# Performance work log

Hardware: AMD Instinct MI355X
Metric: run time of the kernel (lower is better)

## Reference

```python
import jax, jax.numpy as jnp
import numpy as np
from jax import lax

HEATMAP_THRESH = 0.1


def _conv(x, w, b, stride=1):
    y = lax.conv_general_dilated(x, w, (stride, stride), 'SAME',
                                 dimension_numbers=('NCHW', 'OIHW', 'NCHW'))
    return y + b[None, :, None, None]


def _maxpool2(x):
    return lax.reduce_window(x, -jnp.inf, lax.max, (1, 1, 2, 2), (1, 1, 2, 2), 'VALID')


def _up2(x):
    return jnp.repeat(jnp.repeat(x, 2, axis=2), 2, axis=3)


def _find_peaks_mask(hm, thresh):
    # Vectorized equivalent of the CPU nested-loop _find_peaks:
    # interior pixel is a peak iff v > thresh and v >= its 4 axial neighbors.
    c = hm[:, :, 1:-1, 1:-1]
    m = ((c > thresh)
         & (c >= hm[:, :, :-2, 1:-1]) & (c >= hm[:, :, 2:, 1:-1])
         & (c >= hm[:, :, 1:-1, :-2]) & (c >= hm[:, :, 1:-1, 2:]))
    return jnp.pad(m, ((0, 0), (0, 0), (1, 1), (1, 1)))  # border never a peak


def _param(key, shape):
    fan_in = int(np.prod(shape[1:]))
    return jax.random.normal(key, shape, jnp.float32) / np.sqrt(fan_in)


_SHAPES = {
    'w_d1': (32, 3, 3, 3), 'w_d2': (64, 32, 3, 3), 'w_bn': (128, 64, 3, 3),
    'w_u1': (64, 192, 3, 3), 'w_u2': (32, 96, 3, 3), 'w_seg': (1, 32, 1, 1),
    'w_p1': (64, 4, 3, 3), 'w_p2': (128, 64, 3, 3),
    'w_hm': (17, 128, 1, 1), 'w_paf': (32, 128, 1, 1),
}


def setup_inputs() -> dict:
    key = jax.random.key(0)
    ks = jax.random.split(key, 1 + len(_SHAPES))
    B, H, W = 8, 384, 384
    inp = {'x': jax.random.normal(ks[0], (B, 3, H, W), jnp.float32)}
    for i, (n, s) in enumerate(_SHAPES.items()):
        inp[n] = _param(ks[i + 1], s)
        inp[n.replace('w_', 'b_')] = jnp.zeros((s[0],), jnp.float32)
    return inp


def _forward(x, w_d1, b_d1, w_d2, b_d2, w_bn, b_bn, w_u1, b_u1, w_u2, b_u2,
             w_seg, b_seg, w_p1, b_p1, w_p2, b_p2, w_hm, b_hm, w_paf, b_paf):
    # --- UNet segmentation ---
    d1 = jax.nn.relu(_conv(x, w_d1, b_d1))                    # [B,32,384,384]
    d2 = jax.nn.relu(_conv(_maxpool2(d1), w_d2, b_d2))        # [B,64,192,192]
    bn = jax.nn.relu(_conv(_maxpool2(d2), w_bn, b_bn))        # [B,128,96,96]
    u1 = jax.nn.relu(_conv(jnp.concatenate([_up2(bn), d2], 1), w_u1, b_u1))  # [B,64,192,192]
    u2 = jax.nn.relu(_conv(jnp.concatenate([_up2(u1), d1], 1), w_u2, b_u2))  # [B,32,384,384]
    seg = _conv(u2, w_seg, b_seg)                             # [B,1,384,384]
    # --- Pose net on image + detached seg logits ---
    xp = jnp.concatenate([x, lax.stop_gradient(seg)], axis=1)  # detach()
    p1 = jax.nn.relu(_conv(xp, w_p1, b_p1, stride=2))          # [B,64,192,192]
    p2 = jax.nn.relu(_conv(p1, w_p2, b_p2, stride=2))          # [B,128,96,96]
    hm = _conv(p2, w_hm, b_hm)                                 # [B,17,96,96]
    paf = _conv(p2, w_paf, b_paf)                              # [B,32,96,96]
    return seg, hm, paf


def reference(x, w_d1, b_d1, w_d2, b_d2, w_bn, b_bn, w_u1, b_u1, w_u2, b_u2,
              w_seg, b_seg, w_p1, b_p1, w_p2, b_p2, w_hm, b_hm, w_paf, b_paf):
    seg, hm, paf = _forward(x, w_d1, b_d1, w_d2, b_d2, w_bn, b_bn, w_u1, b_u1,
                            w_u2, b_u2, w_seg, b_seg, w_p1, b_p1, w_p2, b_p2,
                            w_hm, b_hm, w_paf, b_paf)
    # jit-friendly replacement for the variable-length python peak lists:
    # boolean mask over [B,K,h,w]; (x,y) coords recoverable via jnp.nonzero offline.
    peaks = _find_peaks_mask(hm, HEATMAP_THRESH)
    return seg, hm, paf, peaks
```

## Files before the change

kernel.cpp:

```cpp
#include <hip/hip_runtime.h>


#define BS 256

typedef _Float16 half8 __attribute__((ext_vector_type(8)));
typedef float floatx4 __attribute__((ext_vector_type(4)));

#define LDSDW 20
#define PLT 6000

__global__ __launch_bounds__(BS) void packw_gen_kernel(
    const float* __restrict__ w, _Float16* __restrict__ bp, int Cin, int Cout)
{
    int total = (Cin >> 5) * 9 * (Cout >> 4) * 64;
    int tid = blockIdx.x * BS + threadIdx.x;
    if (tid >= total) return;
    int lane = tid & 63;
    int t = tid >> 6;
    int NTl = Cout >> 4;
    int nt = t % NTl; t /= NTl;
    int tap = t % 9;
    int chunk = t / 9;
    int q = lane >> 4, n = lane & 15;
    int co = nt * 16 + n;
    _Float16* ph = bp + (size_t)tid * 8;
    _Float16* pl = bp + (size_t)total * 8 + (size_t)tid * 8;
#pragma unroll
    for (int j = 0; j < 8; ++j) {
        int ci = chunk * 32 + q * 8 + j;
        float v = w[((size_t)co * Cin + ci) * 9 + tap];
        _Float16 h = (_Float16)v;
        ph[j] = h;
        pl[j] = (_Float16)(v - (float)h);
    }
}

__global__ __launch_bounds__(BS) void packw_1x1_kernel(
    const float* __restrict__ w, _Float16* __restrict__ bp, int Cin, int NTl, int Cout)
{
    int total = (Cin >> 5) * NTl * 64;
    int tid = blockIdx.x * BS + threadIdx.x;
    if (tid >= total) return;
    int lane = tid & 63;
    int t = tid >> 6;
    int nt = t % NTl;
    int chunk = t / NTl;
    int q = lane >> 4, n = lane & 15;
    int co = nt * 16 + n;
    _Float16* ph = bp + (size_t)tid * 8;
    _Float16* pl = bp + (size_t)total * 8 + (size_t)tid * 8;
#pragma unroll
    for (int j = 0; j < 8; ++j) {
        int ci = chunk * 32 + q * 8 + j;
        float v = (co < Cout) ? w[(size_t)co * Cin + ci] : 0.f;
        _Float16 h = (_Float16)v;
        ph[j] = h;
        pl[j] = (_Float16)(v - (float)h);
    }
}

template <int CHUNKS, int NT, int HH, int WW>
__global__ __launch_bounds__(BS) void conv3x3_mfma_kernel(
    const float* __restrict__ in_,
    const _Float16* __restrict__ bp,
    const float* __restrict__ bias,
    float* __restrict__ out)
{
    constexpr int PL = 4 * 34 * LDSDW;
    constexpr int EPI = 64 * NT * 16;
    constexpr int LDS_DW = (2 * PL > EPI) ? 2 * PL : EPI;
    __shared__ unsigned int lds[LDS_DW];

    int xblks = WW / 32;
    int b = blockIdx.x;
    int xb = b % xblks; b /= xblks;
    int yp = b % (HH / 2);
    int n  = b / (HH / 2);
    int y0 = yp * 2;
    int x0 = xb * 32;

    int tid = threadIdx.x;
    int lane = tid & 63, wv = tid >> 6;
    int m = lane & 15, q = lane >> 4;
    int lrow = wv >> 1;
    int lx   = (wv & 1) * 16;

    floatx4 acc[NT];
#pragma unroll
    for (int nt = 0; nt < NT; ++nt) acc[nt] = (floatx4){0.f, 0.f, 0.f, 0.f};

    const int planeW = CHUNKS * 9 * NT * 64 * 8;

    for (int chunk = 0; chunk < CHUNKS; ++chunk) {
        __syncthreads();
        for (int e = tid; e < 4 * 34 * 4; e += BS) {
            int xi = e % 34;
            int rest = e / 34;
            int oct = rest & 3;
            int row = rest >> 2;
            int iy = y0 - 1 + row, gx = x0 - 1 + xi;
            bool ok = (iy >= 0 && iy < HH && gx >= 0 && gx < WW);
            const float* gp = in_ +
                ((size_t)(n * (CHUNKS * 32) + chunk * 32 + oct * 8) * HH + iy) * WW + gx;
            half8 hv, lv;
#pragma unroll
            for (int j = 0; j < 8; ++j) {
                float v = ok ? gp[(size_t)j * HH * WW] : 0.f;
                _Float16 h = (_Float16)v;
                hv[j] = h;
                lv[j] = (_Float16)(v - (float)h);
            }
            int base = (row * 34 + xi) * LDSDW + oct * 4;
            *(half8*)((char*)lds + (size_t)base * 4) = hv;
            *(half8*)((char*)lds + ((size_t)PL + base) * 4) = lv;
        }
        __syncthreads();
#pragma unroll
        for (int ky = 0; ky < 3; ++ky) {
#pragma unroll
            for (int kx = 0; kx < 3; ++kx) {
                int row = lrow + ky;
                int xi  = lx + m + kx;
                int adw = (row * 34 + xi) * LDSDW + q * 4;
                half8 ah = *(const half8*)((const char*)lds + (size_t)adw * 4);
                half8 al = *(const half8*)((const char*)lds + ((size_t)PL + adw) * 4);
                int tap = ky * 3 + kx;
                const _Float16* bpp = bp + ((size_t)(chunk * 9 + tap) * NT) * 64 * 8;
#pragma unroll
                for (int nt = 0; nt < NT; ++nt) {
                    half8 bh = *(const half8*)(bpp + ((size_t)nt * 64 + lane) * 8);
                    half8 bl = *(const half8*)(bpp + planeW + ((size_t)nt * 64 + lane) * 8);
                    acc[nt] = __builtin_amdgcn_mfma_f32_16x16x32_f16(ah, bh, acc[nt], 0, 0, 0);
                    acc[nt] = __builtin_amdgcn_mfma_f32_16x16x32_f16(ah, bl, acc[nt], 0, 0, 0);
                    acc[nt] = __builtin_amdgcn_mfma_f32_16x16x32_f16(al, bh, acc[nt], 0, 0, 0);
                }
            }
        }
    }

    __syncthreads();
#pragma unroll
    for (int nt = 0; nt < NT; ++nt) {
#pragma unroll
        for (int r = 0; r < 4; ++r) {
            int co = nt * 16 + m;
            int pxl = wv * 16 + q * 4 + r;
            ((float*)lds)[co * 64 + pxl] = acc[nt][r];
        }
    }
    __syncthreads();
    {
        constexpr int thPerCo = 256 / (NT * 16);
        constexpr int pxPerTh = 64 / thPerCo;
        int co = tid / thPerCo;
        int sub = tid % thPerCo;
        int pxb = sub * pxPerTh;
        float bb = bias[co];
#pragma unroll
        for (int u = 0; u < pxPerTh; u += 4) {
            int p = pxb + u;
            int row = y0 + (p >> 5), xx = x0 + (p & 31);
            const float* lp = (const float*)lds + co * 64 + p;
            float4 vv = *(const float4*)lp;
            vv.x = fmaxf(vv.x + bb, 0.f);
            vv.y = fmaxf(vv.y + bb, 0.f);
            vv.z = fmaxf(vv.z + bb, 0.f);
            vv.w = fmaxf(vv.w + bb, 0.f);
            *(float4*)(out + ((size_t)(n * NT * 16 + co) * HH + row) * WW + xx) = vv;
        }
    }
}

template <int CHUNKS, int NT, int WI>
__global__ __launch_bounds__(BS) void conv3x3s2_mfma_kernel(
    const float* __restrict__ in_,
    const _Float16* __restrict__ bp,
    const float* __restrict__ bias,
    float* __restrict__ out)
{
    constexpr int WO = WI / 2;
    constexpr int PLs = 5 * 68 * LDSDW;
    constexpr int EPI = 64 * NT * 16;
    constexpr int LDS_DW = (2 * PLs > EPI) ? 2 * PLs : EPI;
    __shared__ unsigned int lds[LDS_DW];

    int xblks = WO / 32;
    int b = blockIdx.x;
    int xb = b % xblks; b /= xblks;
    int yp = b % (WO / 2);
    int n  = b / (WO / 2);
    int y0 = yp * 2;
    int x0 = xb * 32;

    int tid = threadIdx.x;
    int lane = tid & 63, wv = tid >> 6;
    int m = lane & 15, q = lane >> 4;
    int lrow = wv >> 1;
    int lx   = (wv & 1) * 16;

    floatx4 acc[NT];
#pragma unroll
    for (int nt = 0; nt < NT; ++nt) acc[nt] = (floatx4){0.f, 0.f, 0.f, 0.f};

    const int planeW = CHUNKS * 9 * NT * 64 * 8;

    for (int chunk = 0; chunk < CHUNKS; ++chunk) {
        __syncthreads();
        for (int e = tid; e < 5 * 68 * 4; e += BS) {
            int xi = e % 68;
            int rest = e / 68;
            int oct = rest & 3;
            int row = rest >> 2;
            int iy = 2 * y0 + row, ix = 2 * x0 + xi;
            bool ok = (xi < 65 && iy < WI && ix < WI);
            const float* gp = in_ +
                ((size_t)(n * (CHUNKS * 32) + chunk * 32 + oct * 8) * WI + iy) * WI + ix;
            half8 hv, lv;
#pragma unroll
            for (int j = 0; j < 8; ++j) {
                float v = ok ? gp[(size_t)j * WI * WI] : 0.f;
                _Float16 h = (_Float16)v;
                hv[j] = h;
                lv[j] = (_Float16)(v - (float)h);
            }
            int pos = (xi & 1) * 34 + (xi >> 1);
            int base = (row * 68 + pos) * LDSDW + oct * 4;
            *(half8*)((char*)lds + (size_t)base * 4) = hv;
            *(half8*)((char*)lds + ((size_t)PLs + base) * 4) = lv;
        }
        __syncthreads();
#pragma unroll
        for (int ky = 0; ky < 3; ++ky) {
#pragma unroll
            for (int kx = 0; kx < 3; ++kx) {
                int row = 2 * lrow + ky;
                int pos = (kx & 1) * 34 + (lx + m) + (kx >> 1);
                int adw = (row * 68 + pos) * LDSDW + q * 4;
                half8 ah = *(const half8*)((const char*)lds + (size_t)adw * 4);
                half8 al = *(const half8*)((const char*)lds + ((size_t)PLs + adw) * 4);
                int tap = ky * 3 + kx;
                const _Float16* bpp = bp + ((size_t)(chunk * 9 + tap) * NT) * 64 * 8;
#pragma unroll
                for (int nt = 0; nt < NT; ++nt) {
                    half8 bh = *(const half8*)(bpp + ((size_t)nt * 64 + lane) * 8);
                    half8 bl = *(const half8*)(bpp + planeW + ((size_t)nt * 64 + lane) * 8);
                    acc[nt] = __builtin_amdgcn_mfma_f32_16x16x32_f16(ah, bh, acc[nt], 0, 0, 0);
                    acc[nt] = __builtin_amdgcn_mfma_f32_16x16x32_f16(ah, bl, acc[nt], 0, 0, 0);
                    acc[nt] = __builtin_amdgcn_mfma_f32_16x16x32_f16(al, bh, acc[nt], 0, 0, 0);
                }
            }
        }
    }

    __syncthreads();
#pragma unroll
    for (int nt = 0; nt < NT; ++nt) {
#pragma unroll
        for (int r = 0; r < 4; ++r) {
            int co = nt * 16 + m;
            int pxl = wv * 16 + q * 4 + r;
            ((float*)lds)[co * 64 + pxl] = acc[nt][r];
        }
    }
    __syncthreads();
    {
        constexpr int thPerCo = 256 / (NT * 16);
        constexpr int pxPerTh = 64 / thPerCo;
        int co = tid / thPerCo;
        int sub = tid % thPerCo;
        int pxb = sub * pxPerTh;
        float bb = bias[co];
#pragma unroll
        for (int u = 0; u < pxPerTh; u += 4) {
            int p = pxb + u;
            int row = y0 + (p >> 5), xx = x0 + (p & 31);
            const float* lp = (const float*)lds + co * 64 + p;
            float4 vv = *(const float4*)lp;
            vv.x = fmaxf(vv.x + bb, 0.f);
            vv.y = fmaxf(vv.y + bb, 0.f);
            vv.z = fmaxf(vv.z + bb, 0.f);
            vv.w = fmaxf(vv.w + bb, 0.f);
            *(float4*)(out + ((size_t)(n * NT * 16 + co) * WO + row) * WO + xx) = vv;
        }
    }
}

template <int CHUNKS, int NT>
__global__ __launch_bounds__(BS) void conv1x1_mfma_kernel(
    const float* __restrict__ in_,
    const _Float16* __restrict__ bp,
    const float* __restrict__ bias,
    float* __restrict__ out,
    int Cout, int HW)
{
    constexpr int PL1 = 64 * LDSDW;
    constexpr int EPI = 64 * NT * 16;
    constexpr int LDS_DW = (2 * PL1 > EPI) ? 2 * PL1 : EPI;
    __shared__ unsigned int lds[LDS_DW];

    int pblks = HW / 64;
    int b = blockIdx.x;
    int pb = b % pblks;
    int n  = b / pblks;
    int sp0 = pb * 64;

    int tid = threadIdx.x;
    int lane = tid & 63, wv = tid >> 6;
    int m = lane & 15, q = lane >> 4;

    floatx4 acc[NT];
#pragma unroll
    for (int nt = 0; nt < NT; ++nt) acc[nt] = (floatx4){0.f, 0.f, 0.f, 0.f};

    const int planeW = CHUNKS * NT * 64 * 8;

    for (int chunk = 0; chunk < CHUNKS; ++chunk) {
        __syncthreads();
        {
            int px = tid & 63;
            int oct = tid >> 6;
            const float* gp = in_ +
                ((size_t)(n * (CHUNKS * 32) + chunk * 32 + oct * 8)) * HW + sp0 + px;
            half8 hv, lv;
#pragma unroll
            for (int j = 0; j < 8; ++j) {
                float v = gp[(size_t)j * HW];
                _Float16 h = (_Float16)v;
                hv[j] = h;
                lv[j] = (_Float16)(v - (float)h);
            }
            int base = px * LDSDW + oct * 4;
            *(half8*)((char*)lds + (size_t)base * 4) = hv;
            *(half8*)((char*)lds + ((size_t)PL1 + base) * 4) = lv;
        }
        __syncthreads();
        {
            int adw = (wv * 16 + m) * LDSDW + q * 4;
            half8 ah = *(const half8*)((const char*)lds + (size_t)adw * 4);
            half8 al = *(const half8*)((const char*)lds + ((size_t)PL1 + adw) * 4);
            const _Float16* bpp = bp + ((size_t)chunk * NT) * 64 * 8;
#pragma unroll
            for (int nt = 0; nt < NT; ++nt) {
                half8 bh = *(const half8*)(bpp + ((size_t)nt * 64 + lane) * 8);
                half8 bl = *(const half8*)(bpp + planeW + ((size_t)nt * 64 + lane) * 8);
                acc[nt] = __builtin_amdgcn_mfma_f32_16x16x32_f16(ah, bh, acc[nt], 0, 0, 0);
                acc[nt] = __builtin_amdgcn_mfma_f32_16x16x32_f16(ah, bl, acc[nt], 0, 0, 0);
                acc[nt] = __builtin_amdgcn_mfma_f32_16x16x32_f16(al, bh, acc[nt], 0, 0, 0);
            }
        }
    }

    __syncthreads();
#pragma unroll
    for (int nt = 0; nt < NT; ++nt) {
#pragma unroll
        for (int r = 0; r < 4; ++r) {
            ((float*)lds)[(nt * 16 + m) * 64 + wv * 16 + q * 4 + r] = acc[nt][r];
        }
    }
    __syncthreads();
    {
        constexpr int thPerCo = 256 / (NT * 16);
        constexpr int pxPerTh = 64 / thPerCo;
        int co = tid / thPerCo;
        int g  = tid % thPerCo;
        if (co < Cout) {
            float bb = bias[co];
            const float* lp = (const float*)lds + co * 64 + g * pxPerTh;
            float* op = out + ((size_t)(n * Cout + co)) * HW + sp0 + g * pxPerTh;
#pragma unroll
            for (int u = 0; u < pxPerTh; u += 4) {
                float4 vv = *(const float4*)(lp + u);
                vv.x += bb; vv.y += bb; vv.z += bb; vv.w += bb;
                *(float4*)(op + u) = vv;
            }
        }
    }
}

__global__ __launch_bounds__(BS) void u1_mfma_kernel(
    const float* __restrict__ bn_,
    const float* __restrict__ d2_,
    const _Float16* __restrict__ bp,
    const float* __restrict__ b_u1,
    float* __restrict__ out)
{
    __shared__ unsigned int lds[2 * PLT];
    const int Ho = 192, Wo = 192;
    int b = blockIdx.x;
    int xb = b % 4; b /= 4;
    int yb = b % 48;
    int n  = b / 48;
    int y0 = yb * 4;
    int x0 = xb * 48;

    int tid = threadIdx.x;
    int lane = tid & 63, wv = tid >> 6;
    int m = lane & 15, q = lane >> 4;
    int yr = y0 + wv;

    floatx4 acc[3][4];
#pragma unroll
    for (int mt = 0; mt < 3; ++mt)
#pragma unroll
        for (int nt = 0; nt < 4; ++nt) acc[mt][nt] = (floatx4){0.f, 0.f, 0.f, 0.f};

    const int hh0 = (y0 - 1) >> 1;
    const int hx0 = (x0 - 1) >> 1;

    for (int chunk = 0; chunk < 6; ++chunk) {
        __syncthreads();
        if (chunk < 4) {
            for (int e = tid; e < 4 * 26 * 4; e += BS) {
                int xi = e % 26;
                int rest = e / 26;
                int oct = rest & 3;
                int row = rest >> 2;
                int hy = hh0 + row, hx = hx0 + xi;
                bool ok = (hy >= 0 && hy < 96 && hx >= 0 && hx < 96);
                const float* gp = bn_ +
                    ((size_t)(n * 128 + chunk * 32 + oct * 8) * 96 + hy) * 96 + hx;
                half8 hv, lv;
#pragma unroll
                for (int j = 0; j < 8; ++j) {
                    float v = ok ? gp[(size_t)j * 96 * 96] : 0.f;
                    _Float16 h = (_Float16)v;
                    hv[j] = h;
                    lv[j] = (_Float16)(v - (float)h);
                }
                int base = (row * 50 + xi) * LDSDW + oct * 4;
                *(half8*)((char*)lds + (size_t)base * 4) = hv;
                *(half8*)((char*)lds + ((size_t)PLT + base) * 4) = lv;
            }
        } else {
            for (int e = tid; e < 6 * 50 * 4; e += BS) {
                int xi = e % 50;
                int rest = e / 50;
                int oct = rest & 3;
                int row = rest >> 2;
                int iy = y0 - 1 + row, gx = x0 - 1 + xi;
                bool ok = (iy >= 0 && iy < Ho && gx >= 0 && gx < Wo);
                const float* gp = d2_ +
                    ((size_t)(n * 64 + (chunk - 4) * 32 + oct * 8) * Ho + iy) * Wo + gx;
                half8 hv, lv;
#pragma unroll
                for (int j = 0; j < 8; ++j) {
                    float v = ok ? gp[(size_t)j * Ho * Wo] : 0.f;
                    _Float16 h = (_Float16)v;
                    hv[j] = h;
                    lv[j] = (_Float16)(v - (float)h);
                }
                int base = (row * 50 + xi) * LDSDW + oct * 4;
                *(half8*)((char*)lds + (size_t)base * 4) = hv;
                *(half8*)((char*)lds + ((size_t)PLT + base) * 4) = lv;
            }
        }
        __syncthreads();
#pragma unroll
        for (int ky = 0; ky < 3; ++ky) {
#pragma unroll
            for (int kx = 0; kx < 3; ++kx) {
                int tap = ky * 3 + kx;
                const _Float16* bpp = bp + ((size_t)(chunk * 9 + tap) * 4) * 64 * 8;
                half8 bh[4], bl[4];
#pragma unroll
                for (int nt = 0; nt < 4; ++nt) {
                    bh[nt] = *(const half8*)(bpp + ((size_t)nt * 64 + lane) * 8);
                    bl[nt] = *(const half8*)(bpp + 110592 + ((size_t)nt * 64 + lane) * 8);
                }
                int row;
                if (chunk < 4) row = ((yr + ky - 1) >> 1) - hh0;
                else           row = wv + ky;
#pragma unroll
                for (int mt = 0; mt < 3; ++mt) {
                    int px = 16 * mt + m;
                    int xi = (chunk < 4) ? (((x0 + px + kx - 1) >> 1) - hx0)
                                         : (px + kx);
                    int adw = (row * 50 + xi) * LDSDW + q * 4;
                    half8 ah = *(const half8*)((const char*)lds + (size_t)adw * 4);
                    half8 al = *(const half8*)((const char*)lds + ((size_t)PLT + adw) * 4);
#pragma unroll
                    for (int nt = 0; nt < 4; ++nt) {
                        acc[mt][nt] = __builtin_amdgcn_mfma_f32_16x16x32_f16(ah, bh[nt], acc[mt][nt], 0, 0, 0);
                        acc[mt][nt] = __builtin_amdgcn_mfma_f32_16x16x32_f16(ah, bl[nt], acc[mt][nt], 0, 0, 0);
                        acc[mt][nt] = __builtin_amdgcn_mfma_f32_16x16x32_f16(al, bh[nt], acc[mt][nt], 0, 0, 0);
                    }
                }
            }
        }
    }

#pragma unroll
    for (int h = 0; h < 2; ++h) {
        __syncthreads();
#pragma unroll
        for (int ntl = 0; ntl < 2; ++ntl) {
#pragma unroll
            for (int mt = 0; mt < 3; ++mt) {
#pragma unroll
                for (int r = 0; r < 4; ++r) {
                    ((float*)lds)[(ntl * 16 + m) * 192 + wv * 48 + 16 * mt + q * 4 + r]
                        = acc[mt][h * 2 + ntl][r];
                }
            }
        }
        __syncthreads();
        {
            int col = tid >> 3;
            int g   = tid & 7;
            int row = g >> 1, xx = (g & 1) * 24;
            int co = h * 32 + col;
            float bb = b_u1[co];
            const float* lp = (const float*)lds + col * 192 + g * 24;
            float* op = out + ((size_t)(n * 64 + co) * Ho + y0 + row) * Wo + x0 + xx;
#pragma unroll
            for (int u = 0; u < 24; u += 4) {
                float4 vv = *(const float4*)(lp + u);
                vv.x = fmaxf(vv.x + bb, 0.f);
                vv.y = fmaxf(vv.y + bb, 0.f);
                vv.z = fmaxf(vv.z + bb, 0.f);
                vv.w = fmaxf(vv.w + bb, 0.f);
                *(float4*)(op + u) = vv;
            }
        }
    }
}

__global__ __launch_bounds__(BS) void u2seg_mfma_kernel(
    const float* __restrict__ u1_,
    const float* __restrict__ d1_,
    const _Float16* __restrict__ bp,
    const float* __restrict__ b_u2,
    const float* __restrict__ w_seg,
    const float* __restrict__ b_seg,
    float* __restrict__ seg)
{
    __shared__ unsigned int lds[2 * PLT];
    const int Ho = 384, Wo = 384;
    int b = blockIdx.x;
    int xb = b % 8; b /= 8;
    int yb = b % 96;
    int n  = b / 96;
    int y0 = yb * 4;
    int x0 = xb * 48;

    int tid = threadIdx.x;
    int lane = tid & 63, wv = tid >> 6;
    int m = lane & 15, q = lane >> 4;
    int yr = y0 + wv;

    floatx4 acc[3][2];
#pragma unroll
    for (int mt = 0; mt < 3; ++mt) {
        acc[mt][0] = (floatx4){0.f, 0.f, 0.f, 0.f};
        acc[mt][1] = (floatx4){0.f, 0.f, 0.f, 0.f};
    }

    const int hh0 = (y0 - 1) >> 1;
    const int hx0 = (x0 - 1) >> 1;

    for (int chunk = 0; chunk < 3; ++chunk) {
        __syncthreads();
        if (chunk < 2) {
            for (int e = tid; e < 4 * 26 * 4; e += BS) {
                int xi = e % 26;
                int rest = e / 26;
                int oct = rest & 3;
                int row = rest >> 2;
                int hy = hh0 + row, hx = hx0 + xi;
                bool ok = (hy >= 0 && hy < 192 && hx >= 0 && hx < 192);
                const float* gp = u1_ +
                    ((size_t)(n * 64 + chunk * 32 + oct * 8) * 192 + hy) * 192 + hx;
                half8 hv, lv;
#pragma unroll
                for (int j = 0; j < 8; ++j) {
                    float v = ok ? gp[(size_t)j * 192 * 192] : 0.f;
                    _Float16 h = (_Float16)v;
                    hv[j] = h;
                    lv[j] = (_Float16)(v - (float)h);
                }
                int base = (row * 50 + xi) * LDSDW + oct * 4;
                *(half8*)((char*)lds + (size_t)base * 4) = hv;
                *(half8*)((char*)lds + ((size_t)PLT + base) * 4) = lv;
            }
        } else {
            for (int e = tid; e < 6 * 50 * 4; e += BS) {
                int xi = e % 50;
                int rest = e / 50;
                int oct = rest & 3;
                int row = rest >> 2;
                int iy = y0 - 1 + row, gx = x0 - 1 + xi;
                bool ok = (iy >= 0 && iy < Ho && gx >= 0 && gx < Wo);
                const float* gp = d1_ +
                    ((size_t)(n * 32 + oct * 8) * Ho + iy) * Wo + gx;
                half8 hv, lv;
#pragma unroll
                for (int j = 0; j < 8; ++j) {
                    float v = ok ? gp[(size_t)j * Ho * Wo] : 0.f;
                    _Float16 h = (_Float16)v;
                    hv[j] = h;
                    lv[j] = (_Float16)(v - (float)h);
                }
                int base = (row * 50 + xi) * LDSDW + oct * 4;
                *(half8*)((char*)lds + (size_t)base * 4) = hv;
                *(half8*)((char*)lds + ((size_t)PLT + base) * 4) = lv;
            }
        }
        __syncthreads();
#pragma unroll
        for (int ky = 0; ky < 3; ++ky) {
#pragma unroll
            for (int kx = 0; kx < 3; ++kx) {
                int tap = ky * 3 + kx;
                const _Float16* bpp = bp + ((size_t)(chunk * 9 + tap) * 2) * 64 * 8;
                half8 bh0 = *(const half8*)(bpp + (size_t)lane * 8);
                half8 bl0 = *(const half8*)(bpp + 27648 + (size_t)lane * 8);
                half8 bh1 = *(const half8*)(bpp + ((size_t)64 + lane) * 8);
                half8 bl1 = *(const half8*)(bpp + 27648 + ((size_t)64 + lane) * 8);
                int row;
                if (chunk < 2) row = ((yr + ky - 1) >> 1) - hh0;
                else           row = wv + ky;
#pragma unroll
                for (int mt = 0; mt < 3; ++mt) {
                    int px = 16 * mt + m;
                    int xi = (chunk < 2) ? (((x0 + px + kx - 1) >> 1) - hx0)
                                         : (px + kx);
                    int adw = (row * 50 + xi) * LDSDW + q * 4;
                    half8 ah = *(const half8*)((const char*)lds + (size_t)adw * 4);
                    half8 al = *(const half8*)((const char*)lds + ((size_t)PLT + adw) * 4);
                    acc[mt][0] = __builtin_amdgcn_mfma_f32_16x16x32_f16(ah, bh0, acc[mt][0], 0, 0, 0);
                    acc[mt][0] = __builtin_amdgcn_mfma_f32_16x16x32_f16(ah, bl0, acc[mt][0], 0, 0, 0);
                    acc[mt][0] = __builtin_amdgcn_mfma_f32_16x16x32_f16(al, bh0, acc[mt][0], 0, 0, 0);
                    acc[mt][1] = __builtin_amdgcn_mfma_f32_16x16x32_f16(ah, bh1, acc[mt][1], 0, 0, 0);
                    acc[mt][1] = __builtin_amdgcn_mfma_f32_16x16x32_f16(ah, bl1, acc[mt][1], 0, 0, 0);
                    acc[mt][1] = __builtin_amdgcn_mfma_f32_16x16x32_f16(al, bh1, acc[mt][1], 0, 0, 0);
                }
            }
        }
    }

    float bb0 = b_u2[m], bb1 = b_u2[16 + m];
    float ws0 = w_seg[m], ws1 = w_seg[16 + m];
    float bseg = b_seg[0];
#pragma unroll
    for (int mt = 0; mt < 3; ++mt) {
        float sr[4];
#pragma unroll
        for (int r = 0; r < 4; ++r) {
            float p = ws0 * fmaxf(acc[mt][0][r] + bb0, 0.f)
                    + ws1 * fmaxf(acc[mt][1][r] + bb1, 0.f);
            p += __shfl_xor(p, 1);
            p += __shfl_xor(p, 2);
            p += __shfl_xor(p, 4);
            p += __shfl_xor(p, 8);
            sr[r] = p + bseg;
        }
        if (m == 0) {
            float4 o; o.x = sr[0]; o.y = sr[1]; o.z = sr[2]; o.w = sr[3];
            *(float4*)(seg + ((size_t)n * Ho + yr) * Wo + x0 + 16 * mt + q * 4) = o;
        }
    }
}


template <int UPA, int TCO>
__global__ __launch_bounds__(BS, 2) void conv3x3_x8_kernel(
    const float* __restrict__ inA, int Ca,
    const float* __restrict__ inB, int Cb,
    const float* __restrict__ w, const float* __restrict__ b,
    float* __restrict__ out,
    int N, int H, int W, int Cout, int do_relu)
{
    const int W8 = W >> 3;
    int idx = blockIdx.x * BS + threadIdx.x;
    int total = N * H * W8;
    if (idx >= total) return;
    int x8 = idx % W8;
    int t  = idx / W8;
    int y  = t % H;
    int n  = t / H;
    int x0 = x8 << 3;
    const int co0 = blockIdx.y * TCO;
    const bool left_ok  = (x0 > 0);
    const bool right_ok = (x0 + 8 < W);
    const int Cin = Ca + Cb;

    float acc[TCO][8];
#pragma unroll
    for (int j = 0; j < TCO; ++j) {
        float bv = b[co0 + j];
#pragma unroll
        for (int p = 0; p < 8; ++p) acc[j][p] = bv;
    }

    for (int ci = 0; ci < Cin; ++ci) {
        float v[3][10];
#pragma unroll
        for (int ky = 0; ky < 3; ++ky) {
            int iy = y + ky - 1;
            if (iy < 0 || iy >= H) {
#pragma unroll
                for (int p = 0; p < 10; ++p) v[ky][p] = 0.f;
                continue;
            }
            if (UPA == 2 && ci < Ca) {
                const float* r = inA + ((size_t)(n * Ca + ci) * (H >> 1) + (iy >> 1)) * (W >> 1);
                int xh = x0 >> 1;
                float sm = left_ok  ? r[xh - 1] : 0.f;
                float4 qq = *(const float4*)(r + xh);
                float s4 = right_ok ? r[xh + 4] : 0.f;
                v[ky][0] = sm;
                v[ky][1] = qq.x; v[ky][2] = qq.x;
                v[ky][3] = qq.y; v[ky][4] = qq.y;
                v[ky][5] = qq.z; v[ky][6] = qq.z;
                v[ky][7] = qq.w; v[ky][8] = qq.w;
                v[ky][9] = s4;
            } else {
                const float* r = (ci < Ca)
                    ? inA + ((size_t)(n * Ca + ci) * H + iy) * W
                    : inB + ((size_t)(n * Cb + (ci - Ca)) * H + iy) * W;
                v[ky][0] = left_ok ? r[x0 - 1] : 0.f;
                float4 q0 = *(const float4*)(r + x0);
                float4 q1 = *(const float4*)(r + x0 + 4);
                v[ky][1] = q0.x; v[ky][2] = q0.y; v[ky][3] = q0.z; v[ky][4] = q0.w;
                v[ky][5] = q1.x; v[ky][6] = q1.y; v[ky][7] = q1.z; v[ky][8] = q1.w;
                v[ky][9] = right_ok ? r[x0 + 8] : 0.f;
            }
        }
#pragma unroll
        for (int j = 0; j < TCO; ++j) {
            const float* wp = w + ((size_t)(co0 + j) * Cin + ci) * 9;
#pragma unroll
            for (int ky = 0; ky < 3; ++ky) {
                float w0 = wp[ky * 3 + 0], w1 = wp[ky * 3 + 1], w2 = wp[ky * 3 + 2];
#pragma unroll
                for (int p = 0; p < 8; ++p)
                    acc[j][p] += w0 * v[ky][p] + w1 * v[ky][p + 1] + w2 * v[ky][p + 2];
            }
        }
    }

#pragma unroll
    for (int j = 0; j < TCO; ++j) {
#pragma unroll
        for (int p = 0; p < 8; ++p)
            if (do_relu) acc[j][p] = fmaxf(acc[j][p], 0.f);
        float* o = out + ((size_t)(n * Cout + co0 + j) * H + y) * W + x0;
        float4 q0; q0.x = acc[j][0]; q0.y = acc[j][1]; q0.z = acc[j][2]; q0.w = acc[j][3];
        float4 q1; q1.x = acc[j][4]; q1.y = acc[j][5]; q1.z = acc[j][6]; q1.w = acc[j][7];
        *(float4*)o = q0;
        *(float4*)(o + 4) = q1;
    }
}

template <int TCO>
__global__ __launch_bounds__(BS) void conv3x3_s2_co_kernel(
    const float* __restrict__ inA, int Ca,
    const float* __restrict__ inB, int Cb,
    const float* __restrict__ w, const float* __restrict__ b,
    float* __restrict__ out,
    int N, int Hi, int Wi, int Cout, int do_relu)
{
    const int Ho = Hi >> 1, Wo = Wi >> 1, Woq = Wo >> 2;
    int idx = blockIdx.x * BS + threadIdx.x;
    int total = N * Ho * Woq;
    if (idx >= total) return;
    int q  = idx % Woq;
    int t  = idx / Woq;
    int oy = t % Ho;
    int n  = t / Ho;
    int ox0 = q << 2;
    int ix0 = ox0 << 1;
    const int co0 = blockIdx.y * TCO;
    const bool right_ok = (ix0 + 8 < Wi);
    const int Cin = Ca + Cb;

    float acc[TCO][4];
#pragma unroll
    for (int j = 0; j < TCO; ++j) {
        float bv = b[co0 + j];
        acc[j][0] = bv; acc[j][1] = bv; acc[j][2] = bv; acc[j][3] = bv;
    }

    for (int ci = 0; ci < Cin; ++ci) {
        const float* base = (ci < Ca)
            ? inA + (size_t)(n * Ca + ci) * Hi * Wi
            : inB + (size_t)(n * Cb + (ci - Ca)) * Hi * Wi;
        float v[3][9];
#pragma unroll
        for (int ky = 0; ky < 3; ++ky) {
            int iy = 2 * oy + ky;
            if (iy >= Hi) {
#pragma unroll
                for (int p = 0; p < 9; ++p) v[ky][p] = 0.f;
                continue;
            }
            const float* r = base + (size_t)iy * Wi + ix0;
            float4 a = *(const float4*)r;
            float4 c = *(const float4*)(r + 4);
            v[ky][0] = a.x; v[ky][1] = a.y; v[ky][2] = a.z; v[ky][3] = a.w;
            v[ky][4] = c.x; v[ky][5] = c.y; v[ky][6] = c.z; v[ky][7] = c.w;
            v[ky][8] = right_ok ? r[8] : 0.f;
        }
#pragma unroll
        for (int j = 0; j < TCO; ++j) {
            const float* wp = w + ((size_t)(co0 + j) * Cin + ci) * 9;
#pragma unroll
            for (int ky = 0; ky < 3; ++ky) {
                float w0 = wp[ky * 3 + 0], w1 = wp[ky * 3 + 1], w2 = wp[ky * 3 + 2];
#pragma unroll
                for (int p = 0; p < 4; ++p)
                    acc[j][p] += w0 * v[ky][2 * p] + w1 * v[ky][2 * p + 1] + w2 * v[ky][2 * p + 2];
            }
        }
    }

#pragma unroll
    for (int j = 0; j < TCO; ++j) {
        float4 o;
        o.x = acc[j][0]; o.y = acc[j][1]; o.z = acc[j][2]; o.w = acc[j][3];
        if (do_relu) {
            o.x = fmaxf(o.x, 0.f); o.y = fmaxf(o.y, 0.f);
            o.z = fmaxf(o.z, 0.f); o.w = fmaxf(o.w, 0.f);
        }
        *(float4*)(out + ((size_t)(n * Cout + co0 + j) * Ho + oy) * Wo + ox0) = o;
    }
}

__global__ __launch_bounds__(BS) void maxpool2_kernel(
    const float* __restrict__ in, float* __restrict__ out, int NC, int H, int W)
{
    int Ho = H >> 1, Wo = W >> 1, Woq = Wo >> 2;
    int idx = blockIdx.x * BS + threadIdx.x;
    int total = NC * Ho * Woq;
    if (idx >= total) return;
    int x4 = idx % Woq;
    int t  = idx / Woq;
    int y  = t % Ho;
    int c  = t / Ho;
    const float* r0 = in + ((size_t)c * H + 2 * y) * W + 8 * x4;
    const float* r1 = r0 + W;
    float4 a0 = *(const float4*)r0;
    float4 a1 = *(const float4*)(r0 + 4);
    float4 b0 = *(const float4*)r1;
    float4 b1 = *(const float4*)(r1 + 4);
    float4 o;
    o.x = fmaxf(fmaxf(a0.x, a0.y), fmaxf(b0.x, b0.y));
    o.y = fmaxf(fmaxf(a0.z, a0.w), fmaxf(b0.z, b0.w));
    o.z = fmaxf(fmaxf(a1.x, a1.y), fmaxf(b1.x, b1.y));
    o.w = fmaxf(fmaxf(a1.z, a1.w), fmaxf(b1.z, b1.w));
    *(float4*)(out + ((size_t)c * Ho + y) * Wo + 4 * x4) = o;
}

__global__ __launch_bounds__(BS) void peaks_kernel(
    const float* __restrict__ hm, float* __restrict__ out,
    int NC, int H, int W, float thresh)
{
    int idx = blockIdx.x * BS + threadIdx.x;
    int total = NC * H * W;
    if (idx >= total) return;
    int x = idx % W;
    int t = idx / W;
    int y = t % H;
    int c = t / H;
    float r = 0.f;
    if (x >= 1 && x < W - 1 && y >= 1 && y < H - 1) {
        const float* base = hm + (size_t)c * H * W;
        float cv = base[y * W + x];
        if (cv > thresh &&
            cv >= base[(y - 1) * W + x] &&
            cv >= base[(y + 1) * W + x] &&
            cv >= base[y * W + (x - 1)] &&
            cv >= base[y * W + (x + 1)])
            r = 1.f;
    }
    out[idx] = r;
}

static inline int nblk(long n) { return (int)((n + BS - 1) / BS); }

extern "C" void kernel_launch(void* const* d_in, const int* in_sizes, int n_in,
                              void* d_out, int out_size, void* d_ws, size_t ws_size,
                              hipStream_t stream)
{
    const float* x     = (const float*)d_in[0];
    const float* w_d1  = (const float*)d_in[1];  const float* b_d1  = (const float*)d_in[2];
    const float* w_d2  = (const float*)d_in[3];  const float* b_d2  = (const float*)d_in[4];
    const float* w_bn  = (const float*)d_in[5];  const float* b_bn  = (const float*)d_in[6];
    const float* w_u1  = (const float*)d_in[7];  const float* b_u1  = (const float*)d_in[8];
    const float* w_u2  = (const float*)d_in[9];  const float* b_u2  = (const float*)d_in[10];
    const float* w_seg = (const float*)d_in[11]; const float* b_seg = (const float*)d_in[12];
    const float* w_p1  = (const float*)d_in[13]; const float* b_p1  = (const float*)d_in[14];
    const float* w_p2  = (const float*)d_in[15]; const float* b_p2  = (const float*)d_in[16];
    const float* w_hm  = (const float*)d_in[17]; const float* b_hm  = (const float*)d_in[18];
    const float* w_paf = (const float*)d_in[19]; const float* b_paf = (const float*)d_in[20];

    const int N = 8, H = 384, W = 384;
    const int H2 = 192, W2 = 192, H4 = 96, W4 = 96;

    float* ws = (float*)d_ws;
    float* u1  = ws;
    float* d1  = ws + 18874368;
    float* d2  = ws + 18874368;
    float* bn  = ws + 37748736;
    float* pd1 = ws;
    float* pd2 = ws + 47185920;
    float* p1  = ws;
    float* p2  = ws + 18874368;

    float* out_seg   = (float*)d_out;
    float* out_hm    = out_seg + 1179648;
    float* out_paf   = out_hm + 1253376;
    float* out_peaks = out_paf + 2359296;
    _Float16* bp_u1  = (_Float16*)(out_seg + 4792320);
    _Float16* bp_u2  = (_Float16*)(out_seg + 4902912);
    _Float16* bp_d2  = (_Float16*)(out_seg + 4930560);
    _Float16* bp_bn  = (_Float16*)(out_seg + 4948992);
    _Float16* bp_p2  = (_Float16*)(out_seg + 5022720);
    _Float16* bp_hm  = (_Float16*)(out_seg + 5096448);
    _Float16* bp_paf = (_Float16*)(out_seg + 5100544);

    packw_gen_kernel<<<nblk(13824), BS, 0, stream>>>(w_u1, bp_u1, 192, 64);
    packw_gen_kernel<<<nblk(3456),  BS, 0, stream>>>(w_u2, bp_u2, 96, 32);
    packw_gen_kernel<<<nblk(2304),  BS, 0, stream>>>(w_d2, bp_d2, 32, 64);
    packw_gen_kernel<<<nblk(9216),  BS, 0, stream>>>(w_bn, bp_bn, 64, 128);
    packw_gen_kernel<<<nblk(9216),  BS, 0, stream>>>(w_p2, bp_p2, 64, 128);
    packw_1x1_kernel<<<nblk(512),   BS, 0, stream>>>(w_hm, bp_hm, 128, 2, 17);
    packw_1x1_kernel<<<nblk(512),   BS, 0, stream>>>(w_paf, bp_paf, 128, 2, 32);
    {
        dim3 g(nblk((long)N * H * (W / 8)), 32 / 8);
        conv3x3_x8_kernel<1, 8><<<g, BS, 0, stream>>>(
            x, 3, nullptr, 0, w_d1, b_d1, d1, N, H, W, 32, 1);
    }
    maxpool2_kernel<<<nblk((long)N * 32 * H2 * (W2 / 4)), BS, 0, stream>>>(d1, pd1, N * 32, H, W);
    conv3x3_mfma_kernel<1, 4, 192, 192><<<8 * 96 * 6, BS, 0, stream>>>(
        pd1, bp_d2, b_d2, d2);
    maxpool2_kernel<<<nblk((long)N * 64 * H4 * (W4 / 4)), BS, 0, stream>>>(d2, pd2, N * 64, H2, W2);
    conv3x3_mfma_kernel<2, 8, 96, 96><<<8 * 48 * 3, BS, 0, stream>>>(
        pd2, bp_bn, b_bn, bn);
    u1_mfma_kernel<<<8 * 48 * 4, BS, 0, stream>>>(bn, d2, bp_u1, b_u1, u1);
    {
        dim3 g(nblk((long)N * H * (W / 8)), 32 / 8);
        conv3x3_x8_kernel<1, 8><<<g, BS, 0, stream>>>(
            x, 3, nullptr, 0, w_d1, b_d1, d1, N, H, W, 32, 1);
    }
    u2seg_mfma_kernel<<<8 * 96 * 8, BS, 0, stream>>>(
        u1, d1, bp_u2, b_u2, w_seg, b_seg, out_seg);
    {
        dim3 g(nblk((long)N * H2 * (W2 / 4)), 64 / 8);
        conv3x3_s2_co_kernel<8><<<g, BS, 0, stream>>>(
            x, 3, out_seg, 1, w_p1, b_p1, p1, N, H, W, 64, 1);
    }
    conv3x3s2_mfma_kernel<2, 8, 192><<<8 * 48 * 3, BS, 0, stream>>>(
        p1, bp_p2, b_p2, p2);
    conv1x1_mfma_kernel<4, 2><<<8 * 144, BS, 0, stream>>>(
        p2, bp_hm, b_hm, out_hm, 17, H4 * W4);
    conv1x1_mfma_kernel<4, 2><<<8 * 144, BS, 0, stream>>>(
        p2, bp_paf, b_paf, out_paf, 32, H4 * W4);
    peaks_kernel<<<nblk((long)N * 17 * H4 * W4), BS, 0, stream>>>(
        out_hm, out_peaks, N * 17, H4, W4, 0.1f);
}
```

Measured before the change: 1.013 ms.

## Store intermediate activations as pre-split fp16 hi/lo in channel-octet layout

Producer kernels (d2, bn, u1, the recomputed d1) now write their activations directly as fp16 high/low split pairs in an NC8HW8 layout. Consumer kernels then load half8 vectors instead of doing eight strided fp32 loads plus a split conversion per element. This removes redundant conversion work and uncoalesced channel-strided reads in the u1 and u2seg staging. In exchange the producer epilogues do more work, the workspace buffers are rearranged, and d2 is written twice (fp32 for maxpool and split for u1).

New measurement: 982.8 us. 1.03x faster.

```diff
diff --git a/kernel.cpp b/kernel.cpp
--- a/kernel.cpp
+++ b/kernel.cpp
@@ -59,12 +59,14 @@
     }
 }
 
-template <int CHUNKS, int NT, int HH, int WW>
+template <int CHUNKS, int NT, int HH, int WW, int OUTMODE>
 __global__ __launch_bounds__(BS) void conv3x3_mfma_kernel(
     const float* __restrict__ in_,
     const _Float16* __restrict__ bp,
     const float* __restrict__ bias,
-    float* __restrict__ out)
+    float* __restrict__ out,
+    _Float16* __restrict__ osph,
+    _Float16* __restrict__ ospl)
 {
     constexpr int PL = 4 * 34 * LDSDW;
     constexpr int EPI = 64 * NT * 16;
@@ -149,7 +151,7 @@
         }
     }
     __syncthreads();
-    {
+    if (OUTMODE != 1) {
         constexpr int thPerCo = 256 / (NT * 16);
         constexpr int pxPerTh = 64 / thPerCo;
         int co = tid / thPerCo;
@@ -169,6 +171,25 @@
             *(float4*)(out + ((size_t)(n * NT * 16 + co) * HH + row) * WW + xx) = vv;
         }
     }
+    if (OUTMODE >= 1) {
+        constexpr int OCTS = NT * 2;
+        for (int it = tid; it < OCTS * 64; it += BS) {
+            int px = it & 63;
+            int oct = it >> 6;
+            int row = y0 + (px >> 5), xx = x0 + (px & 31);
+            half8 hv, lv;
+#pragma unroll
+            for (int j = 0; j < 8; ++j) {
+                float v = fmaxf(((float*)lds)[(oct * 8 + j) * 64 + px] + bias[oct * 8 + j], 0.f);
+                _Float16 hh = (_Float16)v;
+                hv[j] = hh;
+                lv[j] = (_Float16)(v - (float)hh);
+            }
+            size_t oaddr = ((size_t)((n * OCTS + oct) * HH + row) * WW + xx) * 8;
+            *(half8*)(osph + oaddr) = hv;
+            *(half8*)(ospl + oaddr) = lv;
+        }
+    }
 }
 
 template <int CHUNKS, int NT, int WI>
@@ -379,11 +400,11 @@
 }
 
 __global__ __launch_bounds__(BS) void u1_mfma_kernel(
-    const float* __restrict__ bn_,
-    const float* __restrict__ d2_,
+    const _Float16* __restrict__ bnh, const _Float16* __restrict__ bnl,
+    const _Float16* __restrict__ d2h, const _Float16* __restrict__ d2l,
     const _Float16* __restrict__ bp,
     const float* __restrict__ b_u1,
-    float* __restrict__ out)
+    _Float16* __restrict__ oh, _Float16* __restrict__ ol_)
 {
     __shared__ unsigned int lds[2 * PLT];
     const int Ho = 192, Wo = 192;
@@ -417,16 +438,11 @@
                 int oct = rest & 3;
                 int row = rest >> 2;
                 int hy = hh0 + row, hx = hx0 + xi;
-                bool ok = (hy >= 0 && hy < 96 && hx >= 0 && hx < 96);
-                const float* gp = bn_ +
-                    ((size_t)(n * 128 + chunk * 32 + oct * 8) * 96 + hy) * 96 + hx;
-                half8 hv, lv;
-#pragma unroll
-                for (int j = 0; j < 8; ++j) {
-                    float v = ok ? gp[(size_t)j * 96 * 96] : 0.f;
-                    _Float16 h = (_Float16)v;
-                    hv[j] = h;
-                    lv[j] = (_Float16)(v - (float)h);
+                half8 hv = {}, lv = {};
+                if (hy >= 0 && hy < 96 && hx >= 0 && hx < 96) {
+                    size_t ga = ((size_t)((n * 16 + chunk * 4 + oct) * 96 + hy) * 96 + hx) * 8;
+                    hv = *(const half8*)(bnh + ga);
+                    lv = *(const half8*)(bnl + ga);
                 }
                 int base = (row * 50 + xi) * LDSDW + oct * 4;
                 *(half8*)((char*)lds + (size_t)base * 4) = hv;
@@ -439,16 +455,11 @@
                 int oct = rest & 3;
                 int row = rest >> 2;
                 int iy = y0 - 1 + row, gx = x0 - 1 + xi;
-                bool ok = (iy >= 0 && iy < Ho && gx >= 0 && gx < Wo);
-                const float* gp = d2_ +
-                    ((size_t)(n * 64 + (chunk - 4) * 32 + oct * 8) * Ho + iy) * Wo + gx;
-                half8 hv, lv;
-#pragma unroll
-                for (int j = 0; j < 8; ++j) {
-                    float v = ok ? gp[(size_t)j * Ho * Wo] : 0.f;
-                    _Float16 h = (_Float16)v;
-                    hv[j] = h;
-                    lv[j] = (_Float16)(v - (float)h);
+                half8 hv = {}, lv = {};
+                if (iy >= 0 && iy < Ho && gx >= 0 && gx < Wo) {
+                    size_t ga = ((size_t)((n * 8 + (chunk - 4) * 4 + oct) * Ho + iy) * Wo + gx) * 8;
+                    hv = *(const half8*)(d2h + ga);
+                    lv = *(const half8*)(d2l + ga);
                 }
                 int base = (row * 50 + xi) * LDSDW + oct * 4;
                 *(half8*)((char*)lds + (size_t)base * 4) = hv;
@@ -505,30 +516,29 @@
             }
         }
         __syncthreads();
-        {
-            int col = tid >> 3;
-            int g   = tid & 7;
-            int row = g >> 1, xx = (g & 1) * 24;
-            int co = h * 32 + col;
-            float bb = b_u1[co];
-            const float* lp = (const float*)lds + col * 192 + g * 24;
-            float* op = out + ((size_t)(n * 64 + co) * Ho + y0 + row) * Wo + x0 + xx;
-#pragma unroll
-            for (int u = 0; u < 24; u += 4) {
-                float4 vv = *(const float4*)(lp + u);
-                vv.x = fmaxf(vv.x + bb, 0.f);
-                vv.y = fmaxf(vv.y + bb, 0.f);
-                vv.z = fmaxf(vv.z + bb, 0.f);
-                vv.w = fmaxf(vv.w + bb, 0.f);
-                *(float4*)(op + u) = vv;
-            }
+        for (int it = tid; it < 4 * 192; it += BS) {
+            int px = it % 192;
+            int ol = it / 192;
+            int row = y0 + px / 48, xx = x0 + px % 48;
+            half8 hv, lv;
+#pragma unroll
+            for (int j = 0; j < 8; ++j) {
+                int col = ol * 8 + j;
+                float v = fmaxf(((float*)lds)[col * 192 + px] + b_u1[h * 32 + col], 0.f);
+                _Float16 hh = (_Float16)v;
+                hv[j] = hh;
+                lv[j] = (_Float16)(v - (float)hh);
+            }
+            size_t oaddr = ((size_t)((n * 8 + h * 4 + ol) * Ho + row) * Wo + xx) * 8;
+            *(half8*)(oh + oaddr) = hv;
+            *(half8*)(ol_ + oaddr) = lv;
         }
     }
 }
 
 __global__ __launch_bounds__(BS) void u2seg_mfma_kernel(
-    const float* __restrict__ u1_,
-    const float* __restrict__ d1_,
+    const _Float16* __restrict__ u1h, const _Float16* __restrict__ u1l,
+    const _Float16* __restrict__ d1h, const _Float16* __restrict__ d1l,
     const _Float16* __restrict__ bp,
     const float* __restrict__ b_u2,
     const float* __restrict__ w_seg,
@@ -568,16 +578,11 @@
                 int oct = rest & 3;
                 int row = rest >> 2;
                 int hy = hh0 + row, hx = hx0 + xi;
-                bool ok = (hy >= 0 && hy < 192 && hx >= 0 && hx < 192);
-                const float* gp = u1_ +
-                    ((size_t)(n * 64 + chunk * 32 + oct * 8) * 192 + hy) * 192 + hx;
-                half8 hv, lv;
-#pragma unroll
-                for (int j = 0; j < 8; ++j) {
-                    float v = ok ? gp[(size_t)j * 192 * 192] : 0.f;
-                    _Float16 h = (_Float16)v;
-                    hv[j] = h;
-                    lv[j] = (_Float16)(v - (float)h);
+                half8 hv = {}, lv = {};
+                if (hy >= 0 && hy < 192 && hx >= 0 && hx < 192) {
+                    size_t ga = ((size_t)((n * 8 + chunk * 4 + oct) * 192 + hy) * 192 + hx) * 8;
+                    hv = *(const half8*)(u1h + ga);
+                    lv = *(const half8*)(u1l + ga);
                 }
                 int base = (row * 50 + xi) * LDSDW + oct * 4;
                 *(half8*)((char*)lds + (size_t)base * 4) = hv;
@@ -590,16 +595,11 @@
                 int oct = rest & 3;
                 int row = rest >> 2;
                 int iy = y0 - 1 + row, gx = x0 - 1 + xi;
-                bool ok = (iy >= 0 && iy < Ho && gx >= 0 && gx < Wo);
-                const float* gp = d1_ +
-                    ((size_t)(n * 32 + oct * 8) * Ho + iy) * Wo + gx;
-                half8 hv, lv;
-#pragma unroll
-                for (int j = 0; j < 8; ++j) {
-                    float v = ok ? gp[(size_t)j * Ho * Wo] : 0.f;
-                    _Float16 h = (_Float16)v;
-                    hv[j] = h;
-                    lv[j] = (_Float16)(v - (float)h);
+                half8 hv = {}, lv = {};
+                if (iy >= 0 && iy < Ho && gx >= 0 && gx < Wo) {
+                    size_t ga = ((size_t)((n * 4 + oct) * Ho + iy) * Wo + gx) * 8;
+                    hv = *(const half8*)(d1h + ga);
+                    lv = *(const half8*)(d1l + ga);
                 }
                 int base = (row * 50 + xi) * LDSDW + oct * 4;
                 *(half8*)((char*)lds + (size_t)base * 4) = hv;
@@ -663,13 +663,14 @@
 }
 
 
-template <int UPA, int TCO>
+template <int UPA, int TCO, int SPLIT>
 __global__ __launch_bounds__(BS, 2) void conv3x3_x8_kernel(
     const float* __restrict__ inA, int Ca,
     const float* __restrict__ inB, int Cb,
     const float* __restrict__ w, const float* __restrict__ b,
     float* __restrict__ out,
-    int N, int H, int W, int Cout, int do_relu)
+    int N, int H, int W, int Cout, int do_relu,
+    _Float16* __restrict__ osph, _Float16* __restrict__ ospl)
 {
     const int W8 = W >> 3;
     int idx = blockIdx.x * BS + threadIdx.x;
@@ -740,16 +741,34 @@
         }
     }
 
-#pragma unroll
-    for (int j = 0; j < TCO; ++j) {
-#pragma unroll
-        for (int p = 0; p < 8; ++p)
-            if (do_relu) acc[j][p] = fmaxf(acc[j][p], 0.f);
-        float* o = out + ((size_t)(n * Cout + co0 + j) * H + y) * W + x0;
-        float4 q0; q0.x = acc[j][0]; q0.y = acc[j][1]; q0.z = acc[j][2]; q0.w = acc[j][3];
-        float4 q1; q1.x = acc[j][4]; q1.y = acc[j][5]; q1.z = acc[j][6]; q1.w = acc[j][7];
-        *(float4*)o = q0;
-        *(float4*)(o + 4) = q1;
+    if (SPLIT) {
+#pragma unroll
+        for (int p = 0; p < 8; ++p) {
+            half8 hv, lv;
+#pragma unroll
+            for (int j = 0; j < 8; ++j) {
+                float v = acc[j][p];
+                if (do_relu) v = fmaxf(v, 0.f);
+                _Float16 hh = (_Float16)v;
+                hv[j] = hh;
+                lv[j] = (_Float16)(v - (float)hh);
+            }
+            size_t oaddr = ((size_t)((n * (Cout >> 3) + (co0 >> 3)) * H + y) * W + x0 + p) * 8;
+            *(half8*)(osph + oaddr) = hv;
+            *(half8*)(ospl + oaddr) = lv;
+        }
+    } else {
+#pragma unroll
+        for (int j = 0; j < TCO; ++j) {
+#pragma unroll
+            for (int p = 0; p < 8; ++p)
+                if (do_relu) acc[j][p] = fmaxf(acc[j][p], 0.f);
+            float* o = out + ((size_t)(n * Cout + co0 + j) * H + y) * W + x0;
+            float4 q0; q0.x = acc[j][0]; q0.y = acc[j][1]; q0.z = acc[j][2]; q0.w = acc[j][3];
+            float4 q1; q1.x = acc[j][4]; q1.y = acc[j][5]; q1.z = acc[j][6]; q1.w = acc[j][7];
+            *(float4*)o = q0;
+            *(float4*)(o + 4) = q1;
+        }
     }
 }
 
@@ -899,14 +918,20 @@
     const int H2 = 192, W2 = 192, H4 = 96, W4 = 96;
 
     float* ws = (float*)d_ws;
-    float* u1  = ws;
-    float* d1  = ws + 18874368;
-    float* d2  = ws + 18874368;
-    float* bn  = ws + 37748736;
-    float* pd1 = ws;
-    float* pd2 = ws + 47185920;
-    float* p1  = ws;
-    float* p2  = ws + 18874368;
+    float* d1   = ws + 18874368;
+    float* pd1  = ws;
+    float* d2f  = ws + 9437184;
+    _Float16* d2sp_h = (_Float16*)(ws + 28311552);
+    _Float16* d2sp_l = (_Float16*)(ws + 37748736);
+    float* pd2  = ws + 47185920;
+    _Float16* bnsp_h = (_Float16*)(ws + 18874368);
+    _Float16* bnsp_l = (_Float16*)(ws + 23592960);
+    _Float16* u1sp_h = (_Float16*)(ws);
+    _Float16* u1sp_l = (_Float16*)(ws + 9437184);
+    _Float16* d1sp_h = (_Float16*)(ws + 18874368);
+    _Float16* d1sp_l = (_Float16*)(ws + 37748736);
+    float* p1   = ws;
+    float* p2   = ws + 18874368;
 
     float* out_seg   = (float*)d_out;
     float* out_hm    = out_seg + 1179648;
@@ -929,23 +954,24 @@
     packw_1x1_kernel<<<nblk(512),   BS, 0, stream>>>(w_paf, bp_paf, 128, 2, 32);
     {
         dim3 g(nblk((long)N * H * (W / 8)), 32 / 8);
-        conv3x3_x8_kernel<1, 8><<<g, BS, 0, stream>>>(
-            x, 3, nullptr, 0, w_d1, b_d1, d1, N, H, W, 32, 1);
+        conv3x3_x8_kernel<1, 8, 0><<<g, BS, 0, stream>>>(
+            x, 3, nullptr, 0, w_d1, b_d1, d1, N, H, W, 32, 1, nullptr, nullptr);
     }
     maxpool2_kernel<<<nblk((long)N * 32 * H2 * (W2 / 4)), BS, 0, stream>>>(d1, pd1, N * 32, H, W);
-    conv3x3_mfma_kernel<1, 4, 192, 192><<<8 * 96 * 6, BS, 0, stream>>>(
-        pd1, bp_d2, b_d2, d2);
-    maxpool2_kernel<<<nblk((long)N * 64 * H4 * (W4 / 4)), BS, 0, stream>>>(d2, pd2, N * 64, H2, W2);
-    conv3x3_mfma_kernel<2, 8, 96, 96><<<8 * 48 * 3, BS, 0, stream>>>(
-        pd2, bp_bn, b_bn, bn);
-    u1_mfma_kernel<<<8 * 48 * 4, BS, 0, stream>>>(bn, d2, bp_u1, b_u1, u1);
+    conv3x3_mfma_kernel<1, 4, 192, 192, 2><<<8 * 96 * 6, BS, 0, stream>>>(
+        pd1, bp_d2, b_d2, d2f, d2sp_h, d2sp_l);
+    maxpool2_kernel<<<nblk((long)N * 64 * H4 * (W4 / 4)), BS, 0, stream>>>(d2f, pd2, N * 64, H2, W2);
+    conv3x3_mfma_kernel<2, 8, 96, 96, 1><<<8 * 48 * 3, BS, 0, stream>>>(
+        pd2, bp_bn, b_bn, nullptr, bnsp_h, bnsp_l);
+    u1_mfma_kernel<<<8 * 48 * 4, BS, 0, stream>>>(
+        bnsp_h, bnsp_l, d2sp_h, d2sp_l, bp_u1, b_u1, u1sp_h, u1sp_l);
     {
         dim3 g(nblk((long)N * H * (W / 8)), 32 / 8);
-        conv3x3_x8_kernel<1, 8><<<g, BS, 0, stream>>>(
-            x, 3, nullptr, 0, w_d1, b_d1, d1, N, H, W, 32, 1);
+        conv3x3_x8_kernel<1, 8, 1><<<g, BS, 0, stream>>>(
+            x, 3, nullptr, 0, w_d1, b_d1, nullptr, N, H, W, 32, 1, d1sp_h, d1sp_l);
     }
     u2seg_mfma_kernel<<<8 * 96 * 8, BS, 0, stream>>>(
-        u1, d1, bp_u2, b_u2, w_seg, b_seg, out_seg);
+        u1sp_h, u1sp_l, d1sp_h, d1sp_l, bp_u2, b_u2, w_seg, b_seg, out_seg);
     {
         dim3 g(nblk((long)N * H2 * (W2 / 4)), 64 / 8);
         conv3x3_s2_co_kernel<8><<<g, BS, 0, stream>>>(
```
